# Performance work log

Measured on AMD Instinct MI355X. Metric: run time of the kernel, lower is better.

The kernel has to match this reference:

```python
import jax, jax.numpy as jnp
import numpy as np

D_MODEL = 1024
N_HEADS = 16
WINDOW = 128
B, N, M = 2, 2048, 2048


def _linear_params(key, d_in, d_out):
    kw, kb = jax.random.split(key)
    lim = 1.0 / np.sqrt(d_in)
    w = jax.random.uniform(kw, (d_out, d_in), jnp.float32, -lim, lim)
    b = jax.random.uniform(kb, (d_out,), jnp.float32, -lim, lim)
    return w, b


def setup_inputs() -> dict:
    key = jax.random.key(0)
    ks = jax.random.split(key, 7)
    queries = jax.random.normal(ks[0], (B, N, D_MODEL), jnp.float32)
    keys = jax.random.normal(ks[1], (B, M, D_MODEL), jnp.float32)
    values = jax.random.normal(ks[2], (B, M, D_MODEL), jnp.float32)
    wq, bq = _linear_params(ks[3], D_MODEL, D_MODEL)
    wk, bk = _linear_params(ks[4], D_MODEL, D_MODEL)
    wv, bv = _linear_params(ks[5], D_MODEL, D_MODEL)
    wo, bo = _linear_params(ks[6], D_MODEL, D_MODEL)
    return {"queries": queries, "keys": keys, "values": values,
            "wq": wq, "bq": bq, "wk": wk, "bk": bk,
            "wv": wv, "bv": bv, "wo": wo, "bo": bo}


def reference(queries, keys, values, wq, bq, wk, bk, wv, bv, wo, bo):
    b, n, d = queries.shape
    m = keys.shape[1]
    h = N_HEADS
    hd = d // h
    scale = hd ** -0.5
    # torch Linear: y = x @ W.T + b
    q = (queries @ wq.T + bq).reshape(b, n, h, hd).transpose(0, 2, 1, 3)  # [B,H,N,hd]
    k = (keys @ wk.T + bk).reshape(b, m, h, hd).transpose(0, 2, 1, 3)     # [B,H,M,hd]
    v = (values @ wv.T + bv).reshape(b, m, h, hd).transpose(0, 2, 1, 3)   # [B,H,M,hd]
    logits = jnp.einsum('bhnd,bhmd->bhnm', q, k) * scale                   # [B,H,N,M]
    qi = jnp.arange(n)[:, None]
    ki = jnp.arange(m)[None, :]
    if m != n:
        ki = (ki.astype(jnp.float32) * n / max(m, 1)).astype(jnp.int32)
    local_mask = jnp.abs(qi - ki) > WINDOW // 2                            # [N,M]
    logits = jnp.where(local_mask[None, None], -jnp.inf, logits)
    attn = jax.nn.softmax(logits, axis=-1)
    out = jnp.einsum('bhnm,bhmd->bhnd', attn, v)                           # [B,H,N,hd]
    out = out.transpose(0, 2, 1, 3).reshape(b, n, d)
    return out @ wo.T + bo
```

## Files before the change

kernel.cpp:

```cpp
#include <hip/hip_runtime.h>
#include <math.h>


#define D_MODEL 1024
#define N_HEADS 16
#define HD      64
#define WHALF   64
#define BATCH   2
#define NQTOK   2048
#define MKTOK   2048

typedef float f32x4 __attribute__((ext_vector_type(4)));
typedef short s16x8 __attribute__((ext_vector_type(8)));
typedef unsigned short u16;

static __device__ __forceinline__ u16 f2bf(float x) {
  unsigned u = __float_as_uint(x);
  unsigned r = (u + 0x7fffu + ((u >> 16) & 1u)) >> 16;
  return (u16)r;
}
static __device__ __forceinline__ float bf2f(u16 h) {
  return __uint_as_float(((unsigned)h) << 16);
}

#define MAT  4194304u
#define WMAT 1048576u

__global__ __launch_bounds__(256)
void cvt_all(const float* __restrict__ q, const float* __restrict__ k,
             const float* __restrict__ v, const float* __restrict__ wq,
             const float* __restrict__ wk, const float* __restrict__ wv,
             const float* __restrict__ wo, u16* __restrict__ W) {
  const unsigned g = blockIdx.x * 256 + threadIdx.x;
  const float* src;
  size_t dbase; unsigned off;
  if (g < 524288u)        { src = q;  dbase = 0;                  off = g; }
  else if (g < 1048576u)  { src = k;  dbase = 2u * MAT;           off = g - 524288u; }
  else if (g < 1572864u)  { src = v;  dbase = 4u * MAT;           off = g - 1048576u; }
  else if (g < 1703936u)  { src = wq; dbase = 6u * (size_t)MAT;               off = g - 1572864u; }
  else if (g < 1835008u)  { src = wk; dbase = 6u * (size_t)MAT + 2u * WMAT;   off = g - 1703936u; }
  else if (g < 1966080u)  { src = wv; dbase = 6u * (size_t)MAT + 4u * WMAT;   off = g - 1835008u; }
  else                    { src = wo; dbase = 6u * (size_t)MAT + 6u * WMAT;   off = g - 1966080u; }
  const size_t stride = (dbase < 6u * (size_t)MAT) ? MAT : WMAT;
  u16* dh = W + dbase;
  u16* dl = dh + stride;
  const size_t e = (size_t)off * 8;
  const float4 v0 = *(const float4*)(src + e);
  const float4 v1 = *(const float4*)(src + e + 4);
  const float xs[8] = {v0.x, v0.y, v0.z, v0.w, v1.x, v1.y, v1.z, v1.w};
  u16 hs[8], ls[8];
#pragma unroll
  for (int i = 0; i < 8; ++i) {
    hs[i] = f2bf(xs[i]);
    ls[i] = f2bf(xs[i] - bf2f(hs[i]));
  }
  uint4 hv, lv;
  hv.x = hs[0] | ((unsigned)hs[1] << 16); hv.y = hs[2] | ((unsigned)hs[3] << 16);
  hv.z = hs[4] | ((unsigned)hs[5] << 16); hv.w = hs[6] | ((unsigned)hs[7] << 16);
  lv.x = ls[0] | ((unsigned)ls[1] << 16); lv.y = ls[2] | ((unsigned)ls[3] << 16);
  lv.z = ls[4] | ((unsigned)ls[5] << 16); lv.w = ls[6] | ((unsigned)ls[7] << 16);
  *(uint4*)(dh + e) = hv;
  *(uint4*)(dl + e) = lv;
}

#define TBM 128
#define TBN 64
#define TBK 32

__global__ __launch_bounds__(256)
void mfma_gemm(const u16* __restrict__ Ah, const u16* __restrict__ Al,
               const u16* __restrict__ Bh, const u16* __restrict__ Bl,
               const float* __restrict__ bias, float* __restrict__ Cf,
               u16* __restrict__ Ch, u16* __restrict__ Cl, int mode) {
  __shared__ u16 smem[12288];
  const int t  = threadIdx.x;
  const int wv = t >> 6;
  const int ln = t & 63;
  const int row0 = blockIdx.x * TBM;
  const int col0 = blockIdx.y * TBN;
  const int wr = wv >> 1, wc = wv & 1;

  f32x4 acc[4][2];
#pragma unroll
  for (int mi = 0; mi < 4; ++mi)
#pragma unroll
    for (int ni = 0; ni < 2; ++ni)
      acc[mi][ni] = (f32x4){0.f, 0.f, 0.f, 0.f};

  auto lds3 = (__attribute__((address_space(3))) u16*)smem;

  for (int kt = 0; kt < D_MODEL / TBK; ++kt) {
    const int kb = kt * TBK;
    if (kt) __syncthreads();
#pragma unroll
    for (int cc = 0; cc < 6; ++cc) {
      const int c = wv * 6 + cc;
      const u16* src;
      int dst, rowg;
      if (c < 8)       { src = Ah; dst = c * 512;               rowg = row0 + c * 16; }
      else if (c < 16) { src = Al; dst = 4096 + (c - 8) * 512;  rowg = row0 + (c - 8) * 16; }
      else if (c < 20) { src = Bh; dst = 8192 + (c - 16) * 512; rowg = col0 + (c - 16) * 16; }
      else             { src = Bl; dst = 10240 + (c - 20) * 512; rowg = col0 + (c - 20) * 16; }
      const u16* g = src + (size_t)(rowg + (ln >> 2)) * D_MODEL + kb + (ln & 3) * 8;
      __builtin_amdgcn_global_load_lds((const __attribute__((address_space(1))) void*)g,
                                       (__attribute__((address_space(3))) void*)(lds3 + dst),
                                       16, 0, 0);
    }
    __syncthreads();

    const int fr = ln & 15;
    const int ks = (ln >> 4) * 8;
    s16x8 a_h[4], a_l[4], b_h[2], b_l[2];
#pragma unroll
    for (int mi = 0; mi < 4; ++mi) {
      const int r = wr * 64 + mi * 16 + fr;
      a_h[mi] = *(const s16x8*)&smem[r * 32 + ks];
      a_l[mi] = *(const s16x8*)&smem[4096 + r * 32 + ks];
    }
#pragma unroll
    for (int ni = 0; ni < 2; ++ni) {
      const int r = wc * 32 + ni * 16 + fr;
      b_h[ni] = *(const s16x8*)&smem[8192 + r * 32 + ks];
      b_l[ni] = *(const s16x8*)&smem[10240 + r * 32 + ks];
    }
#pragma unroll
    for (int mi = 0; mi < 4; ++mi)
#pragma unroll
      for (int ni = 0; ni < 2; ++ni) {
        acc[mi][ni] = __builtin_amdgcn_mfma_f32_16x16x32_bf16(a_h[mi], b_h[ni], acc[mi][ni], 0, 0, 0);
        acc[mi][ni] = __builtin_amdgcn_mfma_f32_16x16x32_bf16(a_h[mi], b_l[ni], acc[mi][ni], 0, 0, 0);
        acc[mi][ni] = __builtin_amdgcn_mfma_f32_16x16x32_bf16(a_l[mi], b_h[ni], acc[mi][ni], 0, 0, 0);
      }
  }

  const int fr = ln & 15, fq = ln >> 4;
  float bval[2];
  bval[0] = bias[col0 + wc * 32 + fr];
  bval[1] = bias[col0 + wc * 32 + 16 + fr];
#pragma unroll
  for (int mi = 0; mi < 4; ++mi)
#pragma unroll
    for (int ni = 0; ni < 2; ++ni)
#pragma unroll
      for (int j = 0; j < 4; ++j) {
        const int r  = row0 + wr * 64 + mi * 16 + fq * 4 + j;
        const int cg = col0 + wc * 32 + ni * 16 + fr;
        const float o = acc[mi][ni][j] + bval[ni];
        if (mode == 0) {
          Cf[(size_t)r * D_MODEL + cg] = o;
        } else {
          size_t idx;
          if (mode == 1) idx = (size_t)r * D_MODEL + cg;
          else           idx = ((size_t)(r >> 11) * D_MODEL + cg) * (size_t)MKTOK + (r & 2047);
          const u16 hb = f2bf(o);
          Ch[idx] = hb;
          Cl[idx] = f2bf(o - bf2f(hb));
        }
      }
}

__global__ __launch_bounds__(256)
void mfma_attn(const u16* __restrict__ Qh, const u16* __restrict__ Ql,
               const u16* __restrict__ Kh, const u16* __restrict__ Kl,
               const u16* __restrict__ Vth, const u16* __restrict__ Vtl,
               u16* __restrict__ AOh, u16* __restrict__ AOl) {
  __shared__ __align__(16) u16 Pbuf[4][2][32 * 40];
  const int t = threadIdx.x, w = t >> 6, ln = t & 63;
  const int fr = ln & 15, fq = ln >> 4;
  int bb = blockIdx.x;
  bb = (bb & 7) * 64 + (bb >> 3);
  const int g  = bb * 4 + w;
  const int qt = g & 63, h = (g >> 6) & 15, b = g >> 10;
  const int q0 = qt * 32;
  const int jlo = (q0 >= WHALF) ? q0 - WHALF : 0;
  const size_t tb = (size_t)b * NQTOK * D_MODEL;
  const int hc = h * HD;

  s16x8 qf[2][2][2];
#pragma unroll
  for (int mt = 0; mt < 2; ++mt)
#pragma unroll
    for (int kt = 0; kt < 2; ++kt) {
      const size_t o = tb + (size_t)(q0 + mt * 16 + fr) * D_MODEL + hc + kt * 32 + fq * 8;
      qf[mt][kt][0] = *(const s16x8*)(Qh + o);
      qf[mt][kt][1] = *(const s16x8*)(Ql + o);
    }

  f32x4 L[2][10];
#pragma unroll
  for (int mt = 0; mt < 2; ++mt)
#pragma unroll
    for (int nt = 0; nt < 10; ++nt) L[mt][nt] = (f32x4){0.f, 0.f, 0.f, 0.f};
#pragma unroll
  for (int nt = 0; nt < 10; ++nt) {
    int jr = jlo + nt * 16 + fr;
    if (jr > MKTOK - 1) jr = MKTOK - 1;
#pragma unroll
    for (int kt = 0; kt < 2; ++kt) {
      const size_t o = tb + (size_t)jr * D_MODEL + hc + kt * 32 + fq * 8;
      const s16x8 kfh = *(const s16x8*)(Kh + o);
      const s16x8 kfl = *(const s16x8*)(Kl + o);
#pragma unroll
      for (int mt = 0; mt < 2; ++mt) {
        L[mt][nt] = __builtin_amdgcn_mfma_f32_16x16x32_bf16(qf[mt][kt][0], kfh, L[mt][nt], 0, 0, 0);
        L[mt][nt] = __builtin_amdgcn_mfma_f32_16x16x32_bf16(qf[mt][kt][0], kfl, L[mt][nt], 0, 0, 0);
        L[mt][nt] = __builtin_amdgcn_mfma_f32_16x16x32_bf16(qf[mt][kt][1], kfh, L[mt][nt], 0, 0, 0);
      }
    }
  }

  float inv[2][4];
#pragma unroll
  for (int mt = 0; mt < 2; ++mt)
#pragma unroll
    for (int rg = 0; rg < 4; ++rg) {
      const int q = q0 + mt * 16 + fq * 4 + rg;
      float mx = -3.0e38f;
#pragma unroll
      for (int nt = 0; nt < 10; ++nt) {
        const int j = jlo + nt * 16 + fr;
        const int d = q - j;
        const bool ok = (d <= WHALF) && (d >= -WHALF) && (j < MKTOK);
        const float lv = ok ? L[mt][nt][rg] * 0.125f : -3.0e38f;
        L[mt][nt][rg] = lv;
        mx = fmaxf(mx, lv);
      }
      mx = fmaxf(mx, __shfl_xor(mx, 1));
      mx = fmaxf(mx, __shfl_xor(mx, 2));
      mx = fmaxf(mx, __shfl_xor(mx, 4));
      mx = fmaxf(mx, __shfl_xor(mx, 8));
      float sm = 0.f;
#pragma unroll
      for (int nt = 0; nt < 10; ++nt) {
        const float lv = L[mt][nt][rg];
        const float e = (lv > -1.0e38f) ? __expf(lv - mx) : 0.f;
        L[mt][nt][rg] = e;
        sm += e;
      }
      sm += __shfl_xor(sm, 1);
      sm += __shfl_xor(sm, 2);
      sm += __shfl_xor(sm, 4);
      sm += __shfl_xor(sm, 8);
      inv[mt][rg] = 1.f / sm;
    }

  f32x4 oacc[2][4];
#pragma unroll
  for (int mt = 0; mt < 2; ++mt)
#pragma unroll
    for (int nt = 0; nt < 4; ++nt) oacc[mt][nt] = (f32x4){0.f, 0.f, 0.f, 0.f};

  u16* ph = &Pbuf[w][0][0];
  u16* pl = &Pbuf[w][1][0];
#pragma unroll
  for (int c = 0; c < 5; ++c) {
    __syncthreads();
#pragma unroll
    for (int mt = 0; mt < 2; ++mt)
#pragma unroll
      for (int half = 0; half < 2; ++half) {
        const int nt = 2 * c + half;
#pragma unroll
        for (int rg = 0; rg < 4; ++rg) {
          const float v = L[mt][nt][rg] * inv[mt][rg];
          const u16 hb = f2bf(v);
          const int idx = (mt * 16 + fq * 4 + rg) * 40 + half * 16 + fr;
          ph[idx] = hb;
          pl[idx] = f2bf(v - bf2f(hb));
        }
      }
    __syncthreads();
#pragma unroll
    for (int mt = 0; mt < 2; ++mt) {
      const s16x8 pfh = *(const s16x8*)&ph[(mt * 16 + fr) * 40 + fq * 8];
      const s16x8 pfl = *(const s16x8*)&pl[(mt * 16 + fr) * 40 + fq * 8];
      int tk = jlo + c * 32 + fq * 8;
      if (tk > MKTOK - 8) tk = MKTOK - 8;
#pragma unroll
      for (int nt = 0; nt < 4; ++nt) {
        const size_t o = ((size_t)b * D_MODEL + hc + nt * 16 + fr) * (size_t)MKTOK + tk;
        const s16x8 vfh = *(const s16x8*)(Vth + o);
        const s16x8 vfl = *(const s16x8*)(Vtl + o);
        oacc[mt][nt] = __builtin_amdgcn_mfma_f32_16x16x32_bf16(pfh, vfh, oacc[mt][nt], 0, 0, 0);
        oacc[mt][nt] = __builtin_amdgcn_mfma_f32_16x16x32_bf16(pfh, vfl, oacc[mt][nt], 0, 0, 0);
        oacc[mt][nt] = __builtin_amdgcn_mfma_f32_16x16x32_bf16(pfl, vfh, oacc[mt][nt], 0, 0, 0);
      }
    }
  }

#pragma unroll
  for (int mt = 0; mt < 2; ++mt)
#pragma unroll
    for (int nt = 0; nt < 4; ++nt)
#pragma unroll
      for (int j = 0; j < 4; ++j) {
        const int q = q0 + mt * 16 + fq * 4 + j;
        const int d = hc + nt * 16 + fr;
        const float o = oacc[mt][nt][j];
        const size_t idx = tb + (size_t)q * D_MODEL + d;
        const u16 hb = f2bf(o);
        AOh[idx] = hb;
        AOl[idx] = f2bf(o - bf2f(hb));
      }
}

#define GBM 128
#define GBN 64
#define GBK 32
#define GSX 132
#define GSW 68

__global__ __launch_bounds__(256)
void proj_gemm(const float* __restrict__ X, const float* __restrict__ W,
               const float* __restrict__ bias, float* __restrict__ C) {
  __shared__ __align__(16) float Xs[GBK][GSX];
  __shared__ __align__(16) float Ws[GBK][GSW];
  const int t   = threadIdx.x;
  const int tx  = t & 15;
  const int ty  = t >> 4;
  const int row0 = blockIdx.x * GBM;
  const int col0 = blockIdx.y * GBN;
  float acc[8][4] = {};
  for (int kt = 0; kt < D_MODEL / GBK; ++kt) {
    const int kbase = kt * GBK;
    __syncthreads();
#pragma unroll
    for (int p = 0; p < 4; ++p) {
      const int idx = t + p * 256;
      const int r = idx >> 3, f = idx & 7;
      const float4 v = *(const float4*)(X + (size_t)(row0 + r) * D_MODEL + kbase + f * 4);
      Xs[f * 4 + 0][r] = v.x; Xs[f * 4 + 1][r] = v.y;
      Xs[f * 4 + 2][r] = v.z; Xs[f * 4 + 3][r] = v.w;
    }
#pragma unroll
    for (int p = 0; p < 2; ++p) {
      const int idx = t + p * 256;
      const int r = idx >> 3, f = idx & 7;
      const float4 v = *(const float4*)(W + (size_t)(col0 + r) * D_MODEL + kbase + f * 4);
      Ws[f * 4 + 0][r] = v.x; Ws[f * 4 + 1][r] = v.y;
      Ws[f * 4 + 2][r] = v.z; Ws[f * 4 + 3][r] = v.w;
    }
    __syncthreads();
#pragma unroll 4
    for (int kk = 0; kk < GBK; ++kk) {
      const float4 a0 = *(const float4*)&Xs[kk][ty * 8];
      const float4 a1 = *(const float4*)&Xs[kk][ty * 8 + 4];
      const float4 b  = *(const float4*)&Ws[kk][tx * 4];
      const float av[8] = {a0.x, a0.y, a0.z, a0.w, a1.x, a1.y, a1.z, a1.w};
      const float bv[4] = {b.x, b.y, b.z, b.w};
#pragma unroll
      for (int i = 0; i < 8; ++i)
#pragma unroll
        for (int j = 0; j < 4; ++j)
          acc[i][j] = fmaf(av[i], bv[j], acc[i][j]);
    }
  }
  const float4 b4 = *(const float4*)(bias + col0 + tx * 4);
#pragma unroll
  for (int i = 0; i < 8; ++i) {
    float4 o;
    o.x = acc[i][0] + b4.x; o.y = acc[i][1] + b4.y;
    o.z = acc[i][2] + b4.z; o.w = acc[i][3] + b4.w;
    *(float4*)(C + (size_t)(row0 + ty * 8 + i) * D_MODEL + col0 + tx * 4) = o;
  }
}

#define QB    32
#define CHUNK 80
#define KS    65
#define PS    161

__global__ __launch_bounds__(256)
void local_attn(const float* __restrict__ Q, const float* __restrict__ K,
                const float* __restrict__ V, float* __restrict__ AO) {
  __shared__ float Qs[QB][KS];
  __shared__ float KVs[CHUNK][KS];
  __shared__ float P[QB][PS];
  __shared__ float inv_s[QB];
  const int t = threadIdx.x;
  const int nqb = NQTOK / QB;
  const int bid = blockIdx.x;
  const int qb  = bid % nqb;
  const int h   = (bid / nqb) % N_HEADS;
  const int b   = bid / (nqb * N_HEADS);
  const int q0  = qb * QB;
  const int j_lo = max(0, q0 - WHALF);
  const int j_hi = min(MKTOK - 1, q0 + QB - 1 + WHALF);
  const int KB   = j_hi - j_lo + 1;
  const float scale = 0.125f;
  const size_t base = (size_t)b * NQTOK * D_MODEL + h * HD;
  const float* Qb = Q + base;
  const float* Kb = K + base;
  const float* Vb = V + base;
  for (int idx = t; idx < QB * 16; idx += 256) {
    const int r = idx >> 4, f = idx & 15;
    const float4 v = *(const float4*)(Qb + (size_t)(q0 + r) * D_MODEL + f * 4);
    Qs[r][f * 4 + 0] = v.x * scale; Qs[r][f * 4 + 1] = v.y * scale;
    Qs[r][f * 4 + 2] = v.z * scale; Qs[r][f * 4 + 3] = v.w * scale;
  }
  const int txk = t & 15;
  const int tyq = t >> 4;
  for (int c = 0; c < 2; ++c) {
    const int jc0 = c * CHUNK;
    const int cnt = min(CHUNK, KB - jc0);
    __syncthreads();
    for (int idx = t; idx < cnt * 16; idx += 256) {
      const int r = idx >> 4, f = idx & 15;
      const float4 v = *(const float4*)(Kb + (size_t)(j_lo + jc0 + r) * D_MODEL + f * 4);
      KVs[r][f * 4 + 0] = v.x; KVs[r][f * 4 + 1] = v.y;
      KVs[r][f * 4 + 2] = v.z; KVs[r][f * 4 + 3] = v.w;
    }
    __syncthreads();
    float acc[2][5] = {};
#pragma unroll 4
    for (int d = 0; d < HD; ++d) {
      const float q0v = Qs[2 * tyq + 0][d];
      const float q1v = Qs[2 * tyq + 1][d];
#pragma unroll
      for (int kc = 0; kc < 5; ++kc) {
        const float kv = KVs[txk * 5 + kc][d];
        acc[0][kc] = fmaf(q0v, kv, acc[0][kc]);
        acc[1][kc] = fmaf(q1v, kv, acc[1][kc]);
      }
    }
#pragma unroll
    for (int qc = 0; qc < 2; ++qc)
#pragma unroll
      for (int kc = 0; kc < 5; ++kc)
        P[2 * tyq + qc][jc0 + txk * 5 + kc] = acc[qc][kc];
  }
  __syncthreads();
  {
    const int q = t >> 3, s8 = t & 7;
    const int qi = q0 + q;
    float mx = -1e30f;
    for (int jj = s8; jj < KB; jj += 8) {
      int diff = qi - (j_lo + jj); if (diff < 0) diff = -diff;
      if (diff <= WHALF) mx = fmaxf(mx, P[q][jj]);
    }
    mx = fmaxf(mx, __shfl_xor(mx, 1));
    mx = fmaxf(mx, __shfl_xor(mx, 2));
    mx = fmaxf(mx, __shfl_xor(mx, 4));
    float sum = 0.f;
    for (int jj = s8; jj < KB; jj += 8) {
      int diff = qi - (j_lo + jj); if (diff < 0) diff = -diff;
      float e = 0.f;
      if (diff <= WHALF) { e = expf(P[q][jj] - mx); sum += e; }
      P[q][jj] = e;
    }
    sum += __shfl_xor(sum, 1);
    sum += __shfl_xor(sum, 2);
    sum += __shfl_xor(sum, 4);
    if (s8 == 0) inv_s[q] = 1.f / sum;
  }
  const int d  = t & 63;
  const int qg = t >> 6;
  float oacc[8] = {};
  for (int c = 0; c < 2; ++c) {
    const int jc0 = c * CHUNK;
    const int cnt = min(CHUNK, KB - jc0);
    __syncthreads();
    for (int idx = t; idx < cnt * 16; idx += 256) {
      const int r = idx >> 4, f = idx & 15;
      const float4 v = *(const float4*)(Vb + (size_t)(j_lo + jc0 + r) * D_MODEL + f * 4);
      KVs[r][f * 4 + 0] = v.x; KVs[r][f * 4 + 1] = v.y;
      KVs[r][f * 4 + 2] = v.z; KVs[r][f * 4 + 3] = v.w;
    }
    __syncthreads();
    for (int jj = 0; jj < cnt; ++jj) {
      const float v = KVs[jj][d];
#pragma unroll
      for (int i = 0; i < 8; ++i)
        oacc[i] = fmaf(P[qg * 8 + i][jc0 + jj], v, oacc[i]);
    }
  }
#pragma unroll
  for (int i = 0; i < 8; ++i) {
    const int q = qg * 8 + i;
    AO[base + (size_t)(q0 + q) * D_MODEL + d] = oacc[i] * inv_s[q];
  }
}

extern "C" void kernel_launch(void* const* d_in, const int* in_sizes, int n_in,
                              void* d_out, int out_size, void* d_ws, size_t ws_size,
                              hipStream_t stream) {
  const float* queries = (const float*)d_in[0];
  const float* keys    = (const float*)d_in[1];
  const float* values  = (const float*)d_in[2];
  const float* wq = (const float*)d_in[3];
  const float* bq = (const float*)d_in[4];
  const float* wk = (const float*)d_in[5];
  const float* bk = (const float*)d_in[6];
  const float* wv = (const float*)d_in[7];
  const float* bv = (const float*)d_in[8];
  const float* wo = (const float*)d_in[9];
  const float* bo = (const float*)d_in[10];
  float* out = (float*)d_out;

  const size_t mat  = MAT;
  const size_t wmat = WMAT;
  const size_t need = 117440512;

  if (ws_size >= need) {
    u16* W = (u16*)d_ws;
    u16* xqh = W;
    u16* xql = xqh + mat;
    u16* xkh = W + 2 * mat;
    u16* xkl = xkh + mat;
    u16* xvh = W + 4 * mat;
    u16* xvl = xvh + mat;
    u16* wgt = W + 6 * mat;
    u16* wqh = wgt;             u16* wql = wgt + wmat;
    u16* wkh = wgt + 2 * wmat;  u16* wkl = wgt + 3 * wmat;
    u16* wvh = wgt + 4 * wmat;  u16* wvl = wgt + 5 * wmat;
    u16* woh = wgt + 6 * wmat;  u16* wol = wgt + 7 * wmat;
    u16* outs = wgt + 8 * wmat;
    u16* qh  = outs;            u16* ql  = outs + mat;
    u16* kh  = outs + 2 * mat;  u16* kl  = outs + 3 * mat;
    u16* vth = outs + 4 * mat;  u16* vtl = outs + 5 * mat;
    u16* aoh = xqh;             u16* aol = xql;

    cvt_all<<<dim3(8192), 256, 0, stream>>>(queries, keys, values, wq, wk, wv, wo, W);

    const dim3 gm(BATCH * NQTOK / TBM, D_MODEL / TBN);
    mfma_gemm<<<gm, 256, 0, stream>>>(xqh, xql, wqh, wql, bq, nullptr, qh, ql, 1);
    mfma_gemm<<<gm, 256, 0, stream>>>(xkh, xkl, wkh, wkl, bk, nullptr, kh, kl, 1);
    mfma_gemm<<<gm, 256, 0, stream>>>(xvh, xvl, wvh, wvl, bv, nullptr, vth, vtl, 2);

    mfma_attn<<<dim3(512), 256, 0, stream>>>(qh, ql, kh, kl, vth, vtl, aoh, aol);

    mfma_gemm<<<gm, 256, 0, stream>>>(aoh, aol, woh, wol, bo, out, nullptr, nullptr, 0);
  } else {
    float* Qws = (float*)d_ws;
    float* Kws = Qws + mat;
    float* Vws = Kws + mat;
    float* AOws = Qws;
    const dim3 gg(BATCH * NQTOK / GBM, D_MODEL / GBN);
    proj_gemm<<<gg, 256, 0, stream>>>(queries, wq, bq, Qws);
    proj_gemm<<<gg, 256, 0, stream>>>(keys,    wk, bk, Kws);
    proj_gemm<<<gg, 256, 0, stream>>>(values,  wv, bv, Vws);
    local_attn<<<dim3(BATCH * N_HEADS * (NQTOK / QB)), 256, 0, stream>>>(Qws, Kws, Vws, AOws);
    proj_gemm<<<gg, 256, 0, stream>>>(AOws, wo, bo, out);
  }
}
```

Baseline: 301.5 us.

## Fuse Q/K/V projection GEMMs into one launch with 128x128 tiles

Replaces three separate projection GEMM launches with a single kernel covering all three, choosing the weight, bias and output layout per block from a batch index. Blocks are remapped with a swizzle, and the tile grows from 128x64 to 128x128, so each wave holds a 4x4 grid of MFMA accumulators and A-tile reuse doubles. This removes two launch overheads and tail effects and cuts redundant A loads. In exchange it uses more LDS and registers, which may lower occupancy. The output GEMM is reduced to an fp32-only epilogue.

New measurement: 297.7 us. No clear change (-1.3%).

```diff
diff --git a/kernel.cpp b/kernel.cpp
--- a/kernel.cpp
+++ b/kernel.cpp
@@ -63,6 +63,106 @@
   *(uint4*)(dl + e) = lv;
 }
 
+__global__ __launch_bounds__(256)
+void mfma_gemm_qkv(u16* __restrict__ W, const float* __restrict__ bq,
+                   const float* __restrict__ bk, const float* __restrict__ bv) {
+  __shared__ u16 smem[16384];
+  const int t  = threadIdx.x;
+  const int wv = t >> 6;
+  const int ln = t & 63;
+  const int wr = wv >> 1, wc = wv & 1;
+
+  int lin = blockIdx.x;
+  lin = (lin & 7) * 96 + (lin >> 3);
+  const int bz   = lin >> 8;
+  const int rem  = lin & 255;
+  const int row0 = (rem & 31) * 128;
+  const int col0 = (rem >> 5) * 128;
+
+  const u16* Ah = W + (size_t)2 * bz * MAT;
+  const u16* Al = Ah + MAT;
+  const u16* Bh = W + 6u * (size_t)MAT + (size_t)2 * bz * WMAT;
+  const u16* Bl = Bh + WMAT;
+  u16* Ch = W + 6u * (size_t)MAT + 8u * (size_t)WMAT + (size_t)2 * bz * MAT;
+  u16* Cl = Ch + MAT;
+  const float* bias = (bz == 0) ? bq : ((bz == 1) ? bk : bv);
+
+  f32x4 acc[4][4];
+#pragma unroll
+  for (int mi = 0; mi < 4; ++mi)
+#pragma unroll
+    for (int ni = 0; ni < 4; ++ni)
+      acc[mi][ni] = (f32x4){0.f, 0.f, 0.f, 0.f};
+
+  auto lds3 = (__attribute__((address_space(3))) u16*)smem;
+
+  for (int kt = 0; kt < D_MODEL / 32; ++kt) {
+    const int kb = kt * 32;
+    if (kt) __syncthreads();
+#pragma unroll
+    for (int cc = 0; cc < 8; ++cc) {
+      const int c = wv * 8 + cc;
+      const u16* src;
+      int dst, rowg;
+      if (c < 8)       { src = Ah; dst = c * 512;                rowg = row0 + c * 16; }
+      else if (c < 16) { src = Al; dst = 4096 + (c - 8) * 512;   rowg = row0 + (c - 8) * 16; }
+      else if (c < 24) { src = Bh; dst = 8192 + (c - 16) * 512;  rowg = col0 + (c - 16) * 16; }
+      else             { src = Bl; dst = 12288 + (c - 24) * 512; rowg = col0 + (c - 24) * 16; }
+      const u16* g = src + (size_t)(rowg + (ln >> 2)) * D_MODEL + kb + (ln & 3) * 8;
+      __builtin_amdgcn_global_load_lds((const __attribute__((address_space(1))) void*)g,
+                                       (__attribute__((address_space(3))) void*)(lds3 + dst),
+                                       16, 0, 0);
+    }
+    __syncthreads();
+
+    const int fr = ln & 15;
+    const int ks = (ln >> 4) * 8;
+    s16x8 a_h[4], a_l[4], b_h[4], b_l[4];
+#pragma unroll
+    for (int mi = 0; mi < 4; ++mi) {
+      const int r = wr * 64 + mi * 16 + fr;
+      a_h[mi] = *(const s16x8*)&smem[r * 32 + ks];
+      a_l[mi] = *(const s16x8*)&smem[4096 + r * 32 + ks];
+    }
+#pragma unroll
+    for (int ni = 0; ni < 4; ++ni) {
+      const int r = wc * 64 + ni * 16 + fr;
+      b_h[ni] = *(const s16x8*)&smem[8192 + r * 32 + ks];
+      b_l[ni] = *(const s16x8*)&smem[12288 + r * 32 + ks];
+    }
+#pragma unroll
+    for (int mi = 0; mi < 4; ++mi)
+#pragma unroll
+      for (int ni = 0; ni < 4; ++ni) {
+        acc[mi][ni] = __builtin_amdgcn_mfma_f32_16x16x32_bf16(a_h[mi], b_h[ni], acc[mi][ni], 0, 0, 0);
+        acc[mi][ni] = __builtin_amdgcn_mfma_f32_16x16x32_bf16(a_h[mi], b_l[ni], acc[mi][ni], 0, 0, 0);
+        acc[mi][ni] = __builtin_amdgcn_mfma_f32_16x16x32_bf16(a_l[mi], b_h[ni], acc[mi][ni], 0, 0, 0);
+      }
+  }
+
+  const int fr = ln & 15, fq = ln >> 4;
+  float bval[4];
+#pragma unroll
+  for (int ni = 0; ni < 4; ++ni)
+    bval[ni] = bias[col0 + wc * 64 + ni * 16 + fr];
+#pragma unroll
+  for (int mi = 0; mi < 4; ++mi)
+#pragma unroll
+    for (int ni = 0; ni < 4; ++ni)
+#pragma unroll
+      for (int j = 0; j < 4; ++j) {
+        const int r  = row0 + wr * 64 + mi * 16 + fq * 4 + j;
+        const int cg = col0 + wc * 64 + ni * 16 + fr;
+        const float o = acc[mi][ni][j] + bval[ni];
+        size_t idx;
+        if (bz != 2) idx = (size_t)r * D_MODEL + cg;
+        else         idx = ((size_t)(r >> 11) * D_MODEL + cg) * (size_t)MKTOK + (r & 2047);
+        const u16 hb = f2bf(o);
+        Ch[idx] = hb;
+        Cl[idx] = f2bf(o - bf2f(hb));
+      }
+}
+
 #define TBM 128
 #define TBN 64
 #define TBK 32
@@ -70,8 +170,7 @@
 __global__ __launch_bounds__(256)
 void mfma_gemm(const u16* __restrict__ Ah, const u16* __restrict__ Al,
                const u16* __restrict__ Bh, const u16* __restrict__ Bl,
-               const float* __restrict__ bias, float* __restrict__ Cf,
-               u16* __restrict__ Ch, u16* __restrict__ Cl, int mode) {
+               const float* __restrict__ bias, float* __restrict__ Cf) {
   __shared__ u16 smem[12288];
   const int t  = threadIdx.x;
   const int wv = t >> 6;
@@ -145,17 +244,7 @@
       for (int j = 0; j < 4; ++j) {
         const int r  = row0 + wr * 64 + mi * 16 + fq * 4 + j;
         const int cg = col0 + wc * 32 + ni * 16 + fr;
-        const float o = acc[mi][ni][j] + bval[ni];
-        if (mode == 0) {
-          Cf[(size_t)r * D_MODEL + cg] = o;
-        } else {
-          size_t idx;
-          if (mode == 1) idx = (size_t)r * D_MODEL + cg;
-          else           idx = ((size_t)(r >> 11) * D_MODEL + cg) * (size_t)MKTOK + (r & 2047);
-          const u16 hb = f2bf(o);
-          Ch[idx] = hb;
-          Cl[idx] = f2bf(o - bf2f(hb));
-        }
+        Cf[(size_t)r * D_MODEL + cg] = acc[mi][ni][j] + bval[ni];
       }
 }
 
@@ -503,33 +592,22 @@
 
   if (ws_size >= need) {
     u16* W = (u16*)d_ws;
-    u16* xqh = W;
-    u16* xql = xqh + mat;
-    u16* xkh = W + 2 * mat;
-    u16* xkl = xkh + mat;
-    u16* xvh = W + 4 * mat;
-    u16* xvl = xvh + mat;
     u16* wgt = W + 6 * mat;
-    u16* wqh = wgt;             u16* wql = wgt + wmat;
-    u16* wkh = wgt + 2 * wmat;  u16* wkl = wgt + 3 * wmat;
-    u16* wvh = wgt + 4 * wmat;  u16* wvl = wgt + 5 * wmat;
     u16* woh = wgt + 6 * wmat;  u16* wol = wgt + 7 * wmat;
     u16* outs = wgt + 8 * wmat;
     u16* qh  = outs;            u16* ql  = outs + mat;
     u16* kh  = outs + 2 * mat;  u16* kl  = outs + 3 * mat;
     u16* vth = outs + 4 * mat;  u16* vtl = outs + 5 * mat;
-    u16* aoh = xqh;             u16* aol = xql;
+    u16* aoh = W;               u16* aol = W + mat;
 
     cvt_all<<<dim3(8192), 256, 0, stream>>>(queries, keys, values, wq, wk, wv, wo, W);
 
-    const dim3 gm(BATCH * NQTOK / TBM, D_MODEL / TBN);
-    mfma_gemm<<<gm, 256, 0, stream>>>(xqh, xql, wqh, wql, bq, nullptr, qh, ql, 1);
-    mfma_gemm<<<gm, 256, 0, stream>>>(xkh, xkl, wkh, wkl, bk, nullptr, kh, kl, 1);
-    mfma_gemm<<<gm, 256, 0, stream>>>(xvh, xvl, wvh, wvl, bv, nullptr, vth, vtl, 2);
+    mfma_gemm_qkv<<<dim3(768), 256, 0, stream>>>(W, bq, bk, bv);
 
     mfma_attn<<<dim3(512), 256, 0, stream>>>(qh, ql, kh, kl, vth, vtl, aoh, aol);
 
-    mfma_gemm<<<gm, 256, 0, stream>>>(aoh, aol, woh, wol, bo, out, nullptr, nullptr, 0);
+    mfma_gemm<<<dim3(BATCH * NQTOK / TBM, D_MODEL / TBN), 256, 0, stream>>>(
+        aoh, aol, woh, wol, bo, out);
   } else {
     float* Qws = (float*)d_ws;
     float* Kws = Qws + mat;
```
